# Kernel tuning notes

Hardware: AMD Instinct MI355X
Metric: run time of the kernel (lower is better)

Reference implementation:

```python
import jax, jax.numpy as jnp
import numpy as np

D = 512          # feature dim
N = 4095         # context length
LMBD = 0.9       # eligibility-trace decay
DIM = 2 * D + 1  # 1025
CTX = N + 1      # 4096


def make_M(n: int, lmbd: float) -> jnp.ndarray:
    # M[row, col] = lmbd**(row-col) for col <= row < n, col < n; last row and
    # last column are all zero (M[-1, -1] explicitly zeroed in the original).
    i = jnp.arange(n, dtype=jnp.int32)
    diff = i[:, None] - i[None, :]
    core = jnp.where(diff >= 0, jnp.float32(lmbd) ** jnp.maximum(diff, 0).astype(jnp.float32), 0.0)
    M = jnp.zeros((n + 1, n + 1), dtype=jnp.float32)
    return M.at[:n, :n].set(core)


def setup_inputs() -> dict:
    key = jax.random.key(0)
    kz, kp, kq = jax.random.split(key, 3)
    Z = jax.random.normal(kz, (DIM, CTX), dtype=jnp.float32)
    # nn.Parameter(torch.empty(...)) is uninitialized in the source; use small
    # random values as stand-ins for trained parameters.
    P = jax.random.normal(kp, (DIM, DIM), dtype=jnp.float32) * 0.02
    Q = jax.random.normal(kq, (DIM, DIM), dtype=jnp.float32) * 0.02
    M = make_M(N, LMBD)
    return {"Z": Z, "P": P, "Q": Q, "M": M}


def reference(Z, P, Q, M):
    # X = Z^T Q Z : (CTX, CTX) bilinear attention scores
    X = jnp.einsum("dn,de,em->nm", Z, Q, Z)
    A = jax.nn.softmax(X, axis=-1)          # activation
    # Z + (1/n) * P @ Z @ M @ A ; contract left-to-right to keep (DIM, CTX) intermediates
    PZ = P @ Z                               # (DIM, CTX)
    PZM = PZ @ M                             # (DIM, CTX), M lower-tri decay
    return Z + (1.0 / N) * (PZM @ A)
```

## Files before the change

### kernel.cpp

```cpp
#include <hip/hip_runtime.h>


#define LMBD 0.9f
#define CTXN 4096
#define DIMN 1025
#define DP 1152

#define KSPLIT 1024
#define PSTRIDE ((size_t)DP * CTXN)

typedef __bf16 bf16x8 __attribute__((ext_vector_type(8)));
typedef float f32x4 __attribute__((ext_vector_type(4)));
typedef long lx2 __attribute__((ext_vector_type(2)));

__device__ __forceinline__ unsigned short f2bf(float f) {
  union { float f; unsigned u; } v; v.f = f;
  unsigned r = v.u + 0x7FFFu + ((v.u >> 16) & 1u);
  return (unsigned short)(r >> 16);
}
__device__ __forceinline__ float bf2f(unsigned short h) {
  union { unsigned u; float f; } v; v.u = ((unsigned)h) << 16;
  return v.f;
}

__device__ __forceinline__ void gld_lds16(const void* g, void* l) {
  __builtin_amdgcn_global_load_lds(
      (const __attribute__((address_space(1))) unsigned int*)g,
      (__attribute__((address_space(3))) unsigned int*)l, 16, 0, 0);
}

template <int MODE, int TM, int TN>
__device__ __forceinline__ void gemm_body(
    const unsigned short* __restrict__ A, const unsigned short* __restrict__ B,
    void* __restrict__ Cout, int K, int lda, int ldb, int ldc, int bi, int bj,
    float* __restrict__ pmax, float* __restrict__ psum) {
  constexpr int FI = TM / 32, FJ = TN / 32;
  __shared__ unsigned short sA[TM * 64];
  __shared__ unsigned short sB[TN * 64];
  const int tid = threadIdx.x;
  const int wave = tid >> 6;
  const int lane = tid & 63;
  const long i0 = (long)bi * TM;
  const long j0 = (long)bj * TN;
  const int wm = (wave & 1) * (TM / 2);
  const int wn = (wave >> 1) * (TN / 2);

  f32x4 acc[FI][FJ] = {};

  const int srow8 = lane >> 3;
  const int s = lane & 7;
  const int mrow = lane & 15;
  const int q2 = lane >> 4;
  const int swz = mrow >> 1;

  for (int k0 = 0; k0 < K; k0 += 64) {
    __syncthreads();
#pragma unroll
    for (int c = 0; c < TM / 32; ++c) {
      const int q = wave * (TM / 32) + c;
      const int r = q * 8 + srow8;
      const int gk = (s - ((r & 15) >> 1)) & 7;
      gld_lds16(A + (i0 + r) * (long)lda + k0 + gk * 8, &sA[q * 512]);
    }
#pragma unroll
    for (int c = 0; c < TN / 32; ++c) {
      const int q = wave * (TN / 32) + c;
      const int r = q * 8 + srow8;
      const int gk = (s - ((r & 15) >> 1)) & 7;
      gld_lds16(B + (j0 + r) * (long)ldb + k0 + gk * 8, &sB[q * 512]);
    }
    __syncthreads();
#pragma unroll
    for (int kk = 0; kk < 2; ++kk) {
      const int slot = ((kk * 4 + q2) + swz) & 7;
      bf16x8 af[FI], bfr[FJ];
#pragma unroll
      for (int i = 0; i < FI; ++i)
        af[i] = *(const bf16x8*)&sA[(wm + i * 16 + mrow) * 64 + slot * 8];
#pragma unroll
      for (int j = 0; j < FJ; ++j)
        bfr[j] = *(const bf16x8*)&sB[(wn + j * 16 + mrow) * 64 + slot * 8];
#pragma unroll
      for (int i = 0; i < FI; ++i)
#pragma unroll
        for (int j = 0; j < FJ; ++j)
          acc[i][j] =
              __builtin_amdgcn_mfma_f32_16x16x32_bf16(af[i], bfr[j], acc[i][j], 0, 0, 0);
    }
  }

  const int lr = (lane >> 4) * 4;
  const int lc = lane & 15;
#pragma unroll
  for (int i = 0; i < FI; ++i) {
#pragma unroll
    for (int j = 0; j < FJ; ++j) {
#pragma unroll
      for (int r = 0; r < 4; ++r) {
        const long row = i0 + wm + i * 16 + lr + r;
        const long col = j0 + wn + j * 16 + lc;
        const float v = acc[i][j][r];
        if (MODE == 1) ((float*)Cout)[row * ldc + col] = v;
        else ((unsigned short*)Cout)[row * ldc + col] = f2bf(v);
      }
    }
  }

  if (MODE == 4) {
    float* sMax = (float*)sA;
    float* sSum = (float*)sB;
    const int k8 = (wave & 1) * 4 + (lane >> 4);
    __syncthreads();
#pragma unroll
    for (int j = 0; j < FJ; ++j) {
      float m = -1e30f;
#pragma unroll
      for (int i = 0; i < FI; ++i)
#pragma unroll
        for (int r = 0; r < 4; ++r) m = fmaxf(m, acc[i][j][r]);
      float sv = 0.f;
#pragma unroll
      for (int i = 0; i < FI; ++i)
#pragma unroll
        for (int r = 0; r < 4; ++r) sv += __expf(acc[i][j][r] - m);
      const int c = wn + j * 16 + lc;
      sMax[c * 8 + k8] = m;
      sSum[c * 8 + k8] = sv;
    }
    __syncthreads();
    if (tid < 128) {
      float m = -1e30f;
#pragma unroll
      for (int k = 0; k < 8; ++k) m = fmaxf(m, sMax[tid * 8 + k]);
      float sv = 0.f;
#pragma unroll
      for (int k = 0; k < 8; ++k) sv += sSum[tid * 8 + k] * __expf(sMax[tid * 8 + k] - m);
      pmax[(size_t)bi * CTXN + j0 + tid] = m;
      psum[(size_t)bi * CTXN + j0 + tid] = sv;
    }
  }
}

__global__ __launch_bounds__(256, 2) void gemm_xt(
    const unsigned short* __restrict__ QZT, const unsigned short* __restrict__ ZbT,
    unsigned short* __restrict__ XT, float* __restrict__ pmax,
    float* __restrict__ psum) {
  gemm_body<4, 128, 128>(QZT, ZbT, XT, DP, DP, DP, CTXN, blockIdx.x, blockIdx.y, pmax,
                         psum);
}

__global__ __launch_bounds__(256, 2) void gemm_dual(
    const unsigned short* __restrict__ ZbT, const unsigned short* __restrict__ Qb,
    unsigned short* __restrict__ QZT, const unsigned short* __restrict__ Pb,
    float* __restrict__ PZ) {
  const unsigned g = blockIdx.x;
  if (g < 576) {
    gemm_body<0, 128, 64>(ZbT, Qb, QZT, DP, DP, DP, DP, g & 31, g >> 5, nullptr,
                          nullptr);
  } else {
    const unsigned h = g - 576;
    gemm_body<1, 64, 128>(Pb, ZbT, PZ, DP, DP, DP, CTXN, h >> 5, h & 31, nullptr,
                          nullptr);
  }
}

__global__ __launch_bounds__(256, 2) void gemm_fp8_splitk(
    const unsigned char* __restrict__ A, const unsigned char* __restrict__ B,
    unsigned short* __restrict__ Cout) {
  __shared__ unsigned char sA[128 * 64];
  __shared__ unsigned char sB[128 * 64];
  const int tid = threadIdx.x;
  const int wave = tid >> 6;
  const int lane = tid & 63;
  const unsigned g = blockIdx.x;
  const unsigned bj = g & 31;
  const unsigned t = g >> 5;
  const unsigned bi = t >> 2;
  const unsigned bz = t & 3;
  const long i0 = (long)bi * 128;
  const long j0 = (long)bj * 128;
  const int wm = (wave & 1) * 64;
  const int wn = (wave >> 1) * 64;
  const int kb = bz * KSPLIT;
  Cout += (size_t)bz * PSTRIDE;

  f32x4 acc[4][4] = {};
  const int srow = lane >> 2;
  const int skc = (((lane & 3) - (lane >> 3)) & 3) * 16;
  const int mrow = lane & 15;
  const int slot = ((((lane >> 4) + (mrow >> 1)) & 3)) * 16;

  for (int k0 = kb; k0 < kb + KSPLIT; k0 += 64) {
    __syncthreads();
#pragma unroll
    for (int c = 0; c < 2; ++c) {
      const int q = wave * 2 + c;
      gld_lds16(A + (i0 + q * 16 + srow) * (long)CTXN + k0 + skc, &sA[q * 1024]);
      gld_lds16(B + (j0 + q * 16 + srow) * (long)CTXN + k0 + skc, &sB[q * 1024]);
    }
    __syncthreads();
    lx2 af[4], bfr[4];
#pragma unroll
    for (int i = 0; i < 4; ++i)
      af[i] = *(const lx2*)&sA[(wm + i * 16 + mrow) * 64 + slot];
#pragma unroll
    for (int j = 0; j < 4; ++j)
      bfr[j] = *(const lx2*)&sB[(wn + j * 16 + mrow) * 64 + slot];
#pragma unroll
    for (int i = 0; i < 4; ++i)
#pragma unroll
      for (int j = 0; j < 4; ++j) {
        acc[i][j] = __builtin_amdgcn_mfma_f32_16x16x32_fp8_fp8(af[i].x, bfr[j].x,
                                                               acc[i][j], 0, 0, 0);
        acc[i][j] = __builtin_amdgcn_mfma_f32_16x16x32_fp8_fp8(af[i].y, bfr[j].y,
                                                               acc[i][j], 0, 0, 0);
      }
  }

  const int lr = (lane >> 4) * 4;
  const int lc = lane & 15;
#pragma unroll
  for (int i = 0; i < 4; ++i)
#pragma unroll
    for (int j = 0; j < 4; ++j)
#pragma unroll
      for (int r = 0; r < 4; ++r) {
        const long row = i0 + wm + i * 16 + lr + r;
        if (row < DIMN)
          Cout[row * (long)CTXN + j0 + wn + j * 16 + lc] = f2bf(acc[i][j][r]);
      }
}

__global__ void reduce_kernel(const unsigned short* __restrict__ Pt,
                              const float* __restrict__ Z, float* __restrict__ out) {
  const size_t idx = ((size_t)blockIdx.x * 256 + threadIdx.x) * 4;
  float ax = 0.f, ay = 0.f, az = 0.f, aw = 0.f;
#pragma unroll
  for (int z = 0; z < 4; ++z) {
    const ushort4 v = *(const ushort4*)&Pt[(size_t)z * PSTRIDE + idx];
    ax += bf2f(v.x); ay += bf2f(v.y); az += bf2f(v.z); aw += bf2f(v.w);
  }
  const f32x4 zv = *(const f32x4*)&Z[idx];
  f32x4 o;
  o[0] = zv[0] + ax * 0.00390625f;
  o[1] = zv[1] + ay * 0.00390625f;
  o[2] = zv[2] + az * 0.00390625f;
  o[3] = zv[3] + aw * 0.00390625f;
  *(f32x4*)&out[idx] = o;
}

__global__ void prep_kernel(const float* __restrict__ Z, const float* __restrict__ Q,
                            const float* __restrict__ P,
                            unsigned short* __restrict__ ZbT,
                            unsigned short* __restrict__ Qb,
                            unsigned short* __restrict__ Pb) {
  __shared__ float tile[32][33];
  const unsigned g = blockIdx.x;
  const int tid = threadIdx.x;
  if (g < 4608) {
    const int n0 = (g & 127) * 32, e0 = (g >> 7) * 32;
    const int tx = tid & 31, ty = tid >> 5;
#pragma unroll
    for (int k = 0; k < 4; ++k) {
      const int e = e0 + ty + k * 8;
      tile[ty + k * 8][tx] = (e < DIMN) ? Z[(size_t)e * CTXN + n0 + tx] : 0.f;
    }
    __syncthreads();
#pragma unroll
    for (int k = 0; k < 4; ++k) {
      const int n = n0 + ty + k * 8;
      ZbT[(size_t)n * DP + e0 + tx] = f2bf(tile[tx][ty + k * 8]);
    }
  } else {
    const unsigned id2 = g - 4608;
    const int mat = id2 >= 1296;
    const float* src = mat ? P : Q;
    unsigned short* dst = mat ? Pb : Qb;
    const unsigned e0 = (id2 - (mat ? 1296u : 0u)) * 1024u + tid * 4u;
    const unsigned r = e0 / 1152u;
    const unsigned c = e0 - r * 1152u;
    ushort4 o;
    o.x = (r < DIMN && c + 0 < DIMN) ? f2bf(src[(size_t)r * DIMN + c + 0]) : 0;
    o.y = (r < DIMN && c + 1 < DIMN) ? f2bf(src[(size_t)r * DIMN + c + 1]) : 0;
    o.z = (r < DIMN && c + 2 < DIMN) ? f2bf(src[(size_t)r * DIMN + c + 2]) : 0;
    o.w = (r < DIMN && c + 3 < DIMN) ? f2bf(src[(size_t)r * DIMN + c + 3]) : 0;
    *(ushort4*)&dst[(size_t)r * DP + c] = o;
  }
}

__global__ void red2_kernel(const float* __restrict__ pmax, const float* __restrict__ psum,
                            float* __restrict__ rowmax, float* __restrict__ inv_l) {
  const int n = blockIdx.x * 256 + threadIdx.x;
  float M = -1e30f;
  for (int c = 0; c < 32; ++c) M = fmaxf(M, pmax[(size_t)c * CTXN + n]);
  float s = 0.f;
  for (int c = 0; c < 32; ++c)
    s += psum[(size_t)c * CTXN + n] * __expf(pmax[(size_t)c * CTXN + n] - M);
  rowmax[n] = M;
  inv_l[n] = 1.0f / (4095.0f * s);
}

__global__ __launch_bounds__(256) void ewscan_kernel(
    const unsigned short* __restrict__ XT, const float* __restrict__ rowmax,
    unsigned int* __restrict__ ET, const float* __restrict__ PZ,
    const float* __restrict__ inv_l, unsigned char* __restrict__ PZMb) {
  __shared__ float sF[256];
  const unsigned g = blockIdx.x;
  const int t = threadIdx.x;
  if (g >= 1152) {
    const size_t idx = ((size_t)(g - 1152) * 256 + t) * 4;
    const ushort4 v = *(const ushort4*)&XT[idx];
    const int n = (int)(idx & 4095);
    const float4 rm = *(const float4*)&rowmax[n];
    unsigned p = __builtin_amdgcn_cvt_pk_fp8_f32(__expf(bf2f(v.x) - rm.x),
                                                 __expf(bf2f(v.y) - rm.y), 0, false);
    p = __builtin_amdgcn_cvt_pk_fp8_f32(__expf(bf2f(v.z) - rm.z),
                                        __expf(bf2f(v.w) - rm.w), p, true);
    ET[idx >> 2] = p;
    return;
  }
  const int d = g;
  const float* row = PZ + (size_t)d * CTXN;
  float x[16];
#pragma unroll
  for (int q = 0; q < 4; ++q) {
    const float4 v = *(const float4*)&row[t * 16 + q * 4];
    x[q * 4 + 0] = v.x; x[q * 4 + 1] = v.y; x[q * 4 + 2] = v.z; x[q * 4 + 3] = v.w;
  }
  if (t == 255) x[15] = 0.f;
  float loc[16];
  float run = 0.f;
#pragma unroll
  for (int i = 15; i >= 0; --i) { run = run * LMBD + x[i]; loc[i] = run; }
  float f = loc[0];
  sF[t] = f;
  __syncthreads();
  float mlt = 0.1853020188851841f;
  for (int step = 1; step < 256; step <<= 1) {
    const float other = (t + step < 256) ? sF[t + step] : 0.f;
    __syncthreads();
    f += mlt * other;
    mlt *= mlt;
    sF[t] = f;
    __syncthreads();
  }
  const float R = (t < 255) ? sF[t + 1] : 0.f;
  float il[16];
#pragma unroll
  for (int q = 0; q < 4; ++q) {
    const float4 v = *(const float4*)&inv_l[t * 16 + q * 4];
    il[q * 4 + 0] = v.x * 256.f; il[q * 4 + 1] = v.y * 256.f;
    il[q * 4 + 2] = v.z * 256.f; il[q * 4 + 3] = v.w * 256.f;
  }
  float o[16];
  float p = 1.f;
#pragma unroll
  for (int i = 15; i >= 0; --i) {
    p *= LMBD;
    o[i] = (loc[i] + p * R) * il[i];
  }
  unsigned w[4];
#pragma unroll
  for (int q = 0; q < 4; ++q) {
    unsigned pk = __builtin_amdgcn_cvt_pk_fp8_f32(o[q * 4 + 0], o[q * 4 + 1], 0, false);
    pk = __builtin_amdgcn_cvt_pk_fp8_f32(o[q * 4 + 2], o[q * 4 + 3], pk, true);
    w[q] = pk;
  }
  *(uint4*)&PZMb[(size_t)d * CTXN + t * 16] = make_uint4(w[0], w[1], w[2], w[3]);
}

extern "C" void kernel_launch(void* const* d_in, const int* in_sizes, int n_in,
                              void* d_out, int out_size, void* d_ws, size_t ws_size,
                              hipStream_t stream) {
  const float* Z = (const float*)d_in[0];
  const float* P = (const float*)d_in[1];
  const float* Q = (const float*)d_in[2];

  char* ws = (char*)d_ws;
  size_t off = 0;
  auto alloc = [&](size_t bytes) {
    void* p = ws + off;
    off += (bytes + 255) & ~(size_t)255;
    return p;
  };
  unsigned char* ET   = (unsigned char*)alloc((size_t)CTXN * CTXN);
  unsigned char* PZMb = (unsigned char*)alloc((size_t)DP * CTXN);
  float* rowmax       = (float*)alloc((size_t)CTXN * 4);
  float* inv_l        = (float*)alloc((size_t)CTXN * 4);
  char* pool = (char*)alloc(0);
  unsigned short* ZbT = (unsigned short*)alloc((size_t)CTXN * DP * 2);
  unsigned short* QZT = (unsigned short*)alloc((size_t)CTXN * DP * 2);
  unsigned short* XT  = (unsigned short*)alloc((size_t)CTXN * CTXN * 2);
  float* PZ           = (float*)alloc((size_t)DP * CTXN * 4);
  unsigned short* Qb  = (unsigned short*)alloc((size_t)DP * DP * 2);
  unsigned short* Pb  = (unsigned short*)alloc((size_t)DP * DP * 2);
  float* pmax         = (float*)alloc((size_t)32 * CTXN * 4);
  float* psum         = (float*)alloc((size_t)32 * CTXN * 4);
  unsigned short* partials = (unsigned short*)pool;
  if (off > ws_size) return;

  prep_kernel<<<7200, 256, 0, stream>>>(Z, Q, P, ZbT, Qb, Pb);

  gemm_dual<<<1152, 256, 0, stream>>>(ZbT, Qb, QZT, Pb, PZ);

  gemm_xt<<<dim3(32, 32), 256, 0, stream>>>(QZT, ZbT, XT, pmax, psum);

  red2_kernel<<<16, 256, 0, stream>>>(pmax, psum, rowmax, inv_l);

  ewscan_kernel<<<17536, 256, 0, stream>>>(XT, rowmax, (unsigned int*)ET, PZ, inv_l,
                                           PZMb);

  gemm_fp8_splitk<<<1152, 256, 0, stream>>>(PZMb, ET, partials);
  reduce_kernel<<<4100, 256, 0, stream>>>(partials, Z, (float*)d_out);
}
```

Before: 247.9 us.

## Fuse softmax-stat and split-K reductions into GEMMs via last-block atomic counters

Removes the separate red2 and reduce kernels. The last block to finish each column strip (or each output tile) now does the cross-block reduction, using atomic counters that prep_kernel zeroes first. The bf16 LDS swizzle is also simplified to a cheaper per-lane index. This saves two kernel launches and their tail idle time, but puts a serialized reduction tail on the last-finishing blocks and relies on acq_rel atomics plus fences for correct ordering.

```diff
diff --git a/kernel.cpp b/kernel.cpp
--- a/kernel.cpp
+++ b/kernel.cpp
@@ -33,7 +33,8 @@
 __device__ __forceinline__ void gemm_body(
     const unsigned short* __restrict__ A, const unsigned short* __restrict__ B,
     void* __restrict__ Cout, int K, int lda, int ldb, int ldc, int bi, int bj,
-    float* __restrict__ pmax, float* __restrict__ psum) {
+    float* __restrict__ pmax, float* __restrict__ psum, float* __restrict__ rowmax,
+    float* __restrict__ inv_l, int* __restrict__ cnt) {
   constexpr int FI = TM / 32, FJ = TN / 32;
   __shared__ unsigned short sA[TM * 64];
   __shared__ unsigned short sB[TN * 64];
@@ -48,31 +49,26 @@
   f32x4 acc[FI][FJ] = {};
 
   const int srow8 = lane >> 3;
-  const int s = lane & 7;
+  const int gk = ((lane & 7) - srow8) & 7;
   const int mrow = lane & 15;
   const int q2 = lane >> 4;
-  const int swz = mrow >> 1;
 
   for (int k0 = 0; k0 < K; k0 += 64) {
     __syncthreads();
 #pragma unroll
     for (int c = 0; c < TM / 32; ++c) {
       const int q = wave * (TM / 32) + c;
-      const int r = q * 8 + srow8;
-      const int gk = (s - ((r & 15) >> 1)) & 7;
-      gld_lds16(A + (i0 + r) * (long)lda + k0 + gk * 8, &sA[q * 512]);
+      gld_lds16(A + (i0 + q * 8 + srow8) * (long)lda + k0 + gk * 8, &sA[q * 512]);
     }
 #pragma unroll
     for (int c = 0; c < TN / 32; ++c) {
       const int q = wave * (TN / 32) + c;
-      const int r = q * 8 + srow8;
-      const int gk = (s - ((r & 15) >> 1)) & 7;
-      gld_lds16(B + (j0 + r) * (long)ldb + k0 + gk * 8, &sB[q * 512]);
+      gld_lds16(B + (j0 + q * 8 + srow8) * (long)ldb + k0 + gk * 8, &sB[q * 512]);
     }
     __syncthreads();
 #pragma unroll
     for (int kk = 0; kk < 2; ++kk) {
-      const int slot = ((kk * 4 + q2) + swz) & 7;
+      const int slot = ((kk * 4 + q2) + mrow) & 7;
       bf16x8 af[FI], bfr[FJ];
 #pragma unroll
       for (int i = 0; i < FI; ++i)
@@ -106,7 +102,7 @@
     }
   }
 
-  if (MODE == 4) {
+  if constexpr (MODE == 4) {
     float* sMax = (float*)sA;
     float* sSum = (float*)sB;
     const int k8 = (wave & 1) * 4 + (lane >> 4);
@@ -138,15 +134,34 @@
       pmax[(size_t)bi * CTXN + j0 + tid] = m;
       psum[(size_t)bi * CTXN + j0 + tid] = sv;
     }
+    __shared__ int sflag;
+    __syncthreads();
+    if (tid == 0) {
+      const int old = __hip_atomic_fetch_add(&cnt[bj], 1, __ATOMIC_ACQ_REL,
+                                             __HIP_MEMORY_SCOPE_AGENT);
+      sflag = (old == 31);
+    }
+    __syncthreads();
+    if (sflag && tid < 128) {
+      __threadfence();
+      const int n = j0 + tid;
+      float M = -1e30f;
+      for (int c = 0; c < 32; ++c) M = fmaxf(M, pmax[(size_t)c * CTXN + n]);
+      float s = 0.f;
+      for (int c = 0; c < 32; ++c)
+        s += psum[(size_t)c * CTXN + n] * __expf(pmax[(size_t)c * CTXN + n] - M);
+      rowmax[n] = M;
+      inv_l[n] = 1.0f / (4095.0f * s);
+    }
   }
 }
 
 __global__ __launch_bounds__(256, 2) void gemm_xt(
     const unsigned short* __restrict__ QZT, const unsigned short* __restrict__ ZbT,
-    unsigned short* __restrict__ XT, float* __restrict__ pmax,
-    float* __restrict__ psum) {
+    unsigned short* __restrict__ XT, float* __restrict__ pmax, float* __restrict__ psum,
+    float* __restrict__ rowmax, float* __restrict__ inv_l, int* __restrict__ cnt) {
   gemm_body<4, 128, 128>(QZT, ZbT, XT, DP, DP, DP, CTXN, blockIdx.x, blockIdx.y, pmax,
-                         psum);
+                         psum, rowmax, inv_l, cnt);
 }
 
 __global__ __launch_bounds__(256, 2) void gemm_dual(
@@ -156,17 +171,18 @@
   const unsigned g = blockIdx.x;
   if (g < 576) {
     gemm_body<0, 128, 64>(ZbT, Qb, QZT, DP, DP, DP, DP, g & 31, g >> 5, nullptr,
-                          nullptr);
+                          nullptr, nullptr, nullptr, nullptr);
   } else {
     const unsigned h = g - 576;
     gemm_body<1, 64, 128>(Pb, ZbT, PZ, DP, DP, DP, CTXN, h >> 5, h & 31, nullptr,
-                          nullptr);
+                          nullptr, nullptr, nullptr, nullptr);
   }
 }
 
 __global__ __launch_bounds__(256, 2) void gemm_fp8_splitk(
     const unsigned char* __restrict__ A, const unsigned char* __restrict__ B,
-    unsigned short* __restrict__ Cout) {
+    unsigned short* __restrict__ part, const float* __restrict__ Z,
+    float* __restrict__ out, int* __restrict__ cnt) {
   __shared__ unsigned char sA[128 * 64];
   __shared__ unsigned char sB[128 * 64];
   const int tid = threadIdx.x;
@@ -182,7 +198,7 @@
   const int wm = (wave & 1) * 64;
   const int wn = (wave >> 1) * 64;
   const int kb = bz * KSPLIT;
-  Cout += (size_t)bz * PSTRIDE;
+  unsigned short* Cout = part + (size_t)bz * PSTRIDE;
 
   f32x4 acc[4][4] = {};
   const int srow = lane >> 2;
@@ -229,34 +245,44 @@
         if (row < DIMN)
           Cout[row * (long)CTXN + j0 + wn + j * 16 + lc] = f2bf(acc[i][j][r]);
       }
-}
-
-__global__ void reduce_kernel(const unsigned short* __restrict__ Pt,
-                              const float* __restrict__ Z, float* __restrict__ out) {
-  const size_t idx = ((size_t)blockIdx.x * 256 + threadIdx.x) * 4;
-  float ax = 0.f, ay = 0.f, az = 0.f, aw = 0.f;
-#pragma unroll
-  for (int z = 0; z < 4; ++z) {
-    const ushort4 v = *(const ushort4*)&Pt[(size_t)z * PSTRIDE + idx];
-    ax += bf2f(v.x); ay += bf2f(v.y); az += bf2f(v.z); aw += bf2f(v.w);
-  }
-  const f32x4 zv = *(const f32x4*)&Z[idx];
-  f32x4 o;
-  o[0] = zv[0] + ax * 0.00390625f;
-  o[1] = zv[1] + ay * 0.00390625f;
-  o[2] = zv[2] + az * 0.00390625f;
-  o[3] = zv[3] + aw * 0.00390625f;
-  *(f32x4*)&out[idx] = o;
+
+  __shared__ int sflag;
+  __syncthreads();
+  if (tid == 0) {
+    const int old = __hip_atomic_fetch_add(&cnt[32 + (int)(bi * 32 + bj)], 1,
+                                           __ATOMIC_ACQ_REL, __HIP_MEMORY_SCOPE_AGENT);
+    sflag = (old == 3);
+  }
+  __syncthreads();
+  if (sflag) {
+    __threadfence();
+#pragma unroll 4
+    for (int e = 0; e < 64; ++e) {
+      const int flat = e * 256 + tid;
+      const long row = i0 + (flat >> 7);
+      if (row < DIMN) {
+        const size_t o = row * (size_t)CTXN + j0 + (flat & 127);
+        float s = 0.f;
+#pragma unroll
+        for (int z = 0; z < 4; ++z) s += bf2f(part[(size_t)z * PSTRIDE + o]);
+        out[o] = Z[o] + s * 0.00390625f;
+      }
+    }
+  }
 }
 
 __global__ void prep_kernel(const float* __restrict__ Z, const float* __restrict__ Q,
                             const float* __restrict__ P,
                             unsigned short* __restrict__ ZbT,
                             unsigned short* __restrict__ Qb,
-                            unsigned short* __restrict__ Pb) {
+                            unsigned short* __restrict__ Pb, int* __restrict__ cnts) {
   __shared__ float tile[32][33];
   const unsigned g = blockIdx.x;
   const int tid = threadIdx.x;
+  if (g < 2) {
+    const int ci = (int)g * 256 + tid;
+    if (ci < 320) cnts[ci] = 0;
+  }
   if (g < 4608) {
     const int n0 = (g & 127) * 32, e0 = (g >> 7) * 32;
     const int tx = tid & 31, ty = tid >> 5;
@@ -286,18 +312,6 @@
     o.w = (r < DIMN && c + 3 < DIMN) ? f2bf(src[(size_t)r * DIMN + c + 3]) : 0;
     *(ushort4*)&dst[(size_t)r * DP + c] = o;
   }
-}
-
-__global__ void red2_kernel(const float* __restrict__ pmax, const float* __restrict__ psum,
-                            float* __restrict__ rowmax, float* __restrict__ inv_l) {
-  const int n = blockIdx.x * 256 + threadIdx.x;
-  float M = -1e30f;
-  for (int c = 0; c < 32; ++c) M = fmaxf(M, pmax[(size_t)c * CTXN + n]);
-  float s = 0.f;
-  for (int c = 0; c < 32; ++c)
-    s += psum[(size_t)c * CTXN + n] * __expf(pmax[(size_t)c * CTXN + n] - M);
-  rowmax[n] = M;
-  inv_l[n] = 1.0f / (4095.0f * s);
 }
 
 __global__ __launch_bounds__(256) void ewscan_kernel(
@@ -387,6 +401,7 @@
   unsigned char* PZMb = (unsigned char*)alloc((size_t)DP * CTXN);
   float* rowmax       = (float*)alloc((size_t)CTXN * 4);
   float* inv_l        = (float*)alloc((size_t)CTXN * 4);
+  int* cnts           = (int*)alloc(320 * 4);
   char* pool = (char*)alloc(0);
   unsigned short* ZbT = (unsigned short*)alloc((size_t)CTXN * DP * 2);
   unsigned short* QZT = (unsigned short*)alloc((size_t)CTXN * DP * 2);
@@ -399,17 +414,15 @@
   unsigned short* partials = (unsigned short*)pool;
   if (off > ws_size) return;
 
-  prep_kernel<<<7200, 256, 0, stream>>>(Z, Q, P, ZbT, Qb, Pb);
+  prep_kernel<<<7200, 256, 0, stream>>>(Z, Q, P, ZbT, Qb, Pb, cnts);
 
   gemm_dual<<<1152, 256, 0, stream>>>(ZbT, Qb, QZT, Pb, PZ);
 
-  gemm_xt<<<dim3(32, 32), 256, 0, stream>>>(QZT, ZbT, XT, pmax, psum);
-
-  red2_kernel<<<16, 256, 0, stream>>>(pmax, psum, rowmax, inv_l);
+  gemm_xt<<<dim3(32, 32), 256, 0, stream>>>(QZT, ZbT, XT, pmax, psum, rowmax, inv_l,
+                                            cnts);
 
   ewscan_kernel<<<17536, 256, 0, stream>>>(XT, rowmax, (unsigned int*)ET, PZ, inv_l,
                                            PZMb);
 
-  gemm_fp8_splitk<<<1152, 256, 0, stream>>>(PZMb, ET, partials);
-  reduce_kernel<<<4100, 256, 0, stream>>>(partials, Z, (float*)d_out);
-}
+  gemm_fp8_splitk<<<1152, 256, 0, stream>>>(PZMb, ET, partials, Z, (float*)d_out, cnts);
+}
```

Measured after the change: 397.4 us. 1.6x slower.
